# Kernel tuning notes

Measured on AMD Instinct MI355X. Metric: run time of the kernel, lower is better.

Reference implementation:

```python
import jax, jax.numpy as jnp
import numpy as np

LAMBDA_REG = 0.1
EPS = 1e-05


def setup_inputs() -> dict:
    key = jax.random.key(0)
    k1, k2, k3 = jax.random.split(key, 3)
    D, DIM, N = 32, 16, 4096
    A_real = jax.random.normal(k1, (D, DIM, DIM), dtype=jnp.float32)
    A_imag = jax.random.normal(k2, (D, DIM, DIM), dtype=jnp.float32)
    X = jax.random.normal(k3, (N, D), dtype=jnp.float32)
    return {"A_real": A_real, "A_imag": A_imag, "X": X}


def reference(A_real, A_imag, X):
    # A: [D, dim, dim] complex operators; X: [N, D] real positions
    A = (A_real + 1j * A_imag).astype(jnp.complex64)
    N, D = X.shape
    dim = A.shape[-1]
    Xc = X.astype(jnp.complex64)
    I = jnp.eye(dim, dtype=jnp.complex64)

    valid = jnp.isfinite(Xc)                      # [N, D]
    valid_e = valid[:, :, None, None]             # [N, D, 1, 1]
    scaled_I = Xc[:, :, None, None] * I           # [N, D, dim, dim]
    A_exp = A[None, :, :, :]                      # [1, D, dim, dim] (broadcast over N)
    scaled_I_clean = jnp.where(valid_e, scaled_I, A_exp)
    H_diff = jnp.where(valid_e, A_exp - scaled_I_clean, 0.0)  # [N, D, dim, dim]

    # 0.5 * sum_d H_diff @ H_diff^H  (Hermitian by construction)
    H = 0.5 * jnp.einsum('ndij,ndkj->nik', H_diff, jnp.conj(H_diff))
    H = H + EPS * I                               # [N, dim, dim]

    eigvals, eigvecs = jnp.linalg.eigh(H)
    psi0 = eigvecs[:, :, 0]                       # ground state, [N, dim]
    phase = psi0[:, 0] / jnp.abs(psi0[:, 0])
    psi0 = psi0 / phase[:, None]
    projector = psi0[:, :, None] * jnp.conj(psi0)[:, None, :]  # [N, dim, dim]

    # Faithful to torch.einsum('ndij,njk->nd', ...): sums over i, j AND k
    position = jnp.einsum('dij,njk->nd', A, projector).real    # [N, D]
    A2 = jnp.matmul(A, A)                                       # [D, dim, dim]
    expectation_A2 = jnp.einsum('dij,njk->nd', A2, projector).real
    variance = jnp.sum(expectation_A2 - position ** 2)

    position_error = jnp.sum((position - X) ** 2)
    loss = (position_error + LAMBDA_REG * variance) / N
    return loss
```

## Files before the change

kernel.cpp:

```cpp
#include <hip/hip_runtime.h>

#define NS 4096
#define DC 32
#define MAXROUND 210
#define CHKIV 8

typedef float v2f __attribute__((ext_vector_type(2)));

#define CFENCE() asm volatile("" ::: "memory")

static __device__ __forceinline__ v2f vswap(v2f b) {
    return __builtin_shufflevector(b, b, 1, 0);
}

static __device__ __forceinline__ float dpp_from_hi(float x) {
    return __int_as_float(__builtin_amdgcn_update_dpp(
        0, __float_as_int(x), 0x101, 0xf, 0xf, true));
}
static __device__ __forceinline__ float dpp_from_lo(float x) {
    return __int_as_float(__builtin_amdgcn_update_dpp(
        0, __float_as_int(x), 0x111, 0xf, 0xf, true));
}
static __device__ __forceinline__ v2f dpp2_from_hi(v2f v) {
    return (v2f){dpp_from_hi(v.x), dpp_from_hi(v.y)};
}
static __device__ __forceinline__ v2f dpp2_from_lo(v2f v) {
    return (v2f){dpp_from_lo(v.x), dpp_from_lo(v.y)};
}

static __device__ __forceinline__ int slot_of(int r, int rr) {
    if (r == 15) return 0;
    int m = r - rr; if (m < 0) m += 15;
    if (m == 0) return 1;
    return (m <= 7) ? 2*m : 31 - 2*m;
}
static __device__ __forceinline__ int pi_next(int s) {
    if (s == 0) return 0;
    if (s == 2) return 1;
    if (!(s & 1)) return s - 2;
    return (s == 15) ? 14 : s + 2;
}
static __device__ __forceinline__ int kmix(int sr) {
    return ((sr >> 1) ^ ((sr & 1) << 2)) & 7;
}
static __device__ __forceinline__ int laddr(int sr, int sc) {
    return (sr << 7) | ((((sc >> 1) ^ kmix(sr)) & 7) << 4) | ((sc & 1) << 3);
}

static __device__ __forceinline__ float4 make_rot(float4 f0, float4 f1) {
    float av = f0.x, dv = f1.z;
    float ab2 = f0.z*f0.z + f0.w*f0.w;
    float c_, s_, er, ei;
    if (ab2 > 1e-60f) {
        float abr = __builtin_amdgcn_rsqf(ab2);
        er = f0.z * abr; ei = f0.w * abr;
        float tau = (dv - av) * (0.5f * abr);
        float den = fabsf(tau) + sqrtf(1.f + tau*tau);
        float tv = __builtin_amdgcn_rcpf(den);
        tv = (tau < 0.f) ? -tv : tv;
        c_ = __builtin_amdgcn_rsqf(1.f + tv*tv);
        s_ = tv * c_;
    } else { c_ = 1.f; s_ = 0.f; er = 1.f; ei = 0.f; }
    return make_float4(c_, s_, er, ei);
}

static __device__ __forceinline__ void rot_quartet(
    float4 fa, float4 fb,
    float4 f0, float4 f1, v2f q11, v2f q12, v2f q21, v2f q22,
    v2f& n11, v2f& n12, v2f& n21, v2f& n22,
    v2f& u11, v2f& u12, v2f& u21, v2f& u22)
{
    v2f h11 = {f0.x, f0.y}, h12 = {f0.z, f0.w};
    v2f h21 = {f1.x, f1.y}, h22 = {f1.z, f1.w};

    const float cb = fb.x, sb = fb.y, ebx = fb.z, eby = fb.w;
    const float sbex = sb*ebx, sbey = sb*eby;
    const float cbex = cb*ebx, cbey = cb*eby;
    const v2f CB  = {cb, cb},      SB  = {sb, sb};
    const v2f P1x = {-sbex,-sbex}, P1y = {-sbey, sbey};
    const v2f Q1x = {cbex, cbex},  Q1y = {cbey,-cbey};
    const float ca = fa.x, sa = fa.y, eax = fa.z, eay = fa.w;
    const float saex = sa*eax, saey = sa*eay;
    const float caex = ca*eax, caey = ca*eay;
    const v2f CA  = {ca, ca},      SA  = {sa, sa};
    const v2f P2x = {-saex,-saex}, P2y = {saey,-saey};
    const v2f Q2x = {caex, caex},  Q2y = {-caey, caey};

    v2f t11 = CB*h11  + P1x*h12 + P1y*vswap(h12);
    v2f t12 = Q1x*h12 + Q1y*vswap(h12) + SB*h11;
    v2f t21 = CB*h21  + P1x*h22 + P1y*vswap(h22);
    v2f t22 = Q1x*h22 + Q1y*vswap(h22) + SB*h21;
    n11 = CA*t11  + P2x*t21 + P2y*vswap(t21);
    n12 = CA*t12  + P2x*t22 + P2y*vswap(t22);
    n21 = Q2x*t21 + Q2y*vswap(t21) + SA*t11;
    n22 = Q2x*t22 + Q2y*vswap(t22) + SA*t12;
    u11 = CB*q11  + P1x*q12 + P1y*vswap(q12);
    u12 = Q1x*q12 + Q1y*vswap(q12) + SB*q11;
    u21 = CB*q21  + P1x*q22 + P1y*vswap(q22);
    u22 = Q1x*q22 + Q1y*vswap(q22) + SB*q21;
}

static __device__ __forceinline__ void v_advance(
    bool b0, bool b7,
    v2f u11, v2f u12, v2f u21, v2f u22,
    v2f& q11, v2f& q12, v2f& q21, v2f& q22)
{
    v2f s11 = dpp2_from_hi(u11);
    v2f s21 = dpp2_from_hi(u21);
    v2f l12 = dpp2_from_lo(u12);
    v2f l22 = dpp2_from_lo(u22);
    q11 = b7 ? u12 : (b0 ? u11 : s11);
    q21 = b7 ? u22 : (b0 ? u21 : s21);
    q12 = b0 ? s11 : l12;
    q22 = b0 ? s21 : l22;
}

__global__ __launch_bounds__(256) void precompute_kernel(
    const float* __restrict__ Ar, const float* __restrict__ Ai,
    float2* __restrict__ S, float2* __restrict__ W,
    float2* __restrict__ cA, float2* __restrict__ cA2,
    float* __restrict__ out)
{
    const int d = blockIdx.x;
    const int t = threadIdx.x;
    if (d == 0 && t == 0) out[0] = 0.f;
    const int i = t >> 4, j = t & 15;
    __shared__ float ar[16][16], ai[16][16], a2r[16][16], a2i[16][16];
    ar[i][j] = Ar[d*256 + t];
    ai[i][j] = Ai[d*256 + t];
    __syncthreads();
    float a2re = 0.f, a2im = 0.f, wre = 0.f, wim = 0.f;
    for (int k = 0; k < 16; ++k) {
        float xr = ar[i][k], xi = ai[i][k];
        a2re += xr*ar[k][j] - xi*ai[k][j];
        a2im += xr*ai[k][j] + xi*ar[k][j];
        wre += xr*ar[j][k] + xi*ai[j][k];
        wim += xi*ar[j][k] - xr*ai[j][k];
    }
    S[d*256 + t] = make_float2(ar[i][j] + ar[j][i], ai[i][j] - ai[j][i]);
    W[d*256 + t] = make_float2(wre, wim);
    a2r[i][j] = a2re; a2i[i][j] = a2im;
    __syncthreads();
    if (t < 16) {
        float sr = 0.f, si = 0.f, s2r = 0.f, s2i = 0.f;
        for (int ii = 0; ii < 16; ++ii) {
            sr  += ar[ii][t];  si  += ai[ii][t];
            s2r += a2r[ii][t]; s2i += a2i[ii][t];
        }
        cA [d*16 + t] = make_float2(sr,  si);
        cA2[d*16 + t] = make_float2(s2r, s2i);
    }
}

__global__ __launch_bounds__(64) void energy_kernel(
    const float* __restrict__ X,
    const float2* __restrict__ S, const float2* __restrict__ W,
    const float2* __restrict__ cA, const float2* __restrict__ cA2,
    float* __restrict__ out)
{
    const int n0 = blockIdx.x * 2;
    const int t = threadIdx.x;
    const int a = t >> 3, b = t & 7;

    __shared__ __align__(16) v2f H[2][256];
    __shared__ float4 csco[2][8];
    __shared__ float4 vS[2][16][8];
    __shared__ float  xS[2][32];
    __shared__ float  diagS[2][16];
    __shared__ v2f    psiS[2][16];
    __shared__ int    midxS[2];

    const float* XA = X + n0*DC;
    const float* XB = X + (n0 + 1)*DC;
    if (t < 32) { xS[0][t] = XA[t]; xS[1][t] = XB[t]; }

    const int sr0 = 2*a, sr1 = 2*a + 1;
    const int sc0 = 2*b, sc1 = 2*b + 1;
    const int rd0 = (sr0 << 7) | (((b ^ kmix(sr0)) & 7) << 4);
    const int rd1 = (sr1 << 7) | (((b ^ kmix(sr1)) & 7) << 4);
    const int pr0 = pi_next(sr0), pr1 = pi_next(sr1);
    const int pc0 = pi_next(sc0), pc1 = pi_next(sc1);
    const int wH00 = laddr(pr0, pc0), wH01 = laddr(pr0, pc1);
    const int wH10 = laddr(pr1, pc0), wH11 = laddr(pr1, pc1);
    const bool diagLane = (a == b);
    const bool b0 = (b == 0), b7 = (b == 7);

    const int j0 = b0 ? 15 : b;
    const int j1 = b0 ? 0  : 15 - b;
    v2f qA11 = {(sr0 == j0) ? 1.f : 0.f, 0.f};
    v2f qA12 = {(sr0 == j1) ? 1.f : 0.f, 0.f};
    v2f qA21 = {(sr1 == j0) ? 1.f : 0.f, 0.f};
    v2f qA22 = {(sr1 == j1) ? 1.f : 0.f, 0.f};
    v2f qB11 = qA11, qB12 = qA12, qB21 = qA21, qB22 = qA22;

    float invTolA, invTolB;
    {
        const int bi = t >> 2, bj = (t & 3) * 4, e0 = t * 4;
        v2f accA[4] = {{0.f,0.f},{0.f,0.f},{0.f,0.f},{0.f,0.f}};
        v2f accB[4] = {{0.f,0.f},{0.f,0.f},{0.f,0.f},{0.f,0.f}};
        float sxa = 0.f, sxb = 0.f;
        for (int d = 0; d < DC; ++d) {
            float xa = XA[d], xb = XB[d];
            sxa += xa*xa; sxb += xb*xb;
            const float4* w4 = (const float4*)(W + d*256 + e0);
            const float4* s4 = (const float4*)(S + d*256 + e0);
            float4 wa = w4[0], wb = w4[1];
            float4 sa = s4[0], sb = s4[1];
            v2f xva = {xa, xa}, xvb = {xb, xb};
            accA[0] += (v2f){wa.x, wa.y} - xva * (v2f){sa.x, sa.y};
            accA[1] += (v2f){wa.z, wa.w} - xva * (v2f){sa.z, sa.w};
            accA[2] += (v2f){wb.x, wb.y} - xva * (v2f){sb.x, sb.y};
            accA[3] += (v2f){wb.z, wb.w} - xva * (v2f){sb.z, sb.w};
            accB[0] += (v2f){wa.x, wa.y} - xvb * (v2f){sa.x, sa.y};
            accB[1] += (v2f){wa.z, wa.w} - xvb * (v2f){sa.z, sa.w};
            accB[2] += (v2f){wb.x, wb.y} - xvb * (v2f){sb.x, sb.y};
            accB[3] += (v2f){wb.z, wb.w} - xvb * (v2f){sb.z, sb.w};
        }
        float sdA = 0.5f*sxa + 1e-5f;
        float sdB = 0.5f*sxb + 1e-5f;
        float nfA = 0.f, nfB = 0.f;
        const int sbi = slot_of(bi, 0);
        #pragma unroll
        for (int u = 0; u < 4; ++u) {
            int j = bj + u;
            v2f hA = 0.5f * accA[u];
            v2f hB = 0.5f * accB[u];
            if (bi == j) { hA.x += sdA; hB.x += sdB; }
            nfA += hA.x*hA.x + hA.y*hA.y;
            nfB += hB.x*hB.x + hB.y*hB.y;
            const int scj = slot_of(j, 0);
            *(v2f*)((char*)H + laddr(sbi, scj)) = hA;
            *(v2f*)((char*)H + 2048 + laddr(sbi, scj)) = hB;
        }
        #pragma unroll
        for (int m = 1; m < 64; m <<= 1) {
            nfA += __shfl_xor(nfA, m);
            nfB += __shfl_xor(nfB, m);
        }
        invTolA = __builtin_amdgcn_rcpf(1e-10f * nfA);
        invTolB = __builtin_amdgcn_rcpf(1e-10f * nfB);
    }
    __syncthreads();

    int rr = 0, iter = 0, chkcd = CHKIV;
    for (;;) {
        const char* Hc = (const char*)H;
        float4 f0A = *(const float4*)(Hc + rd0);
        float4 f1A = *(const float4*)(Hc + rd1);
        float4 f0B = *(const float4*)(Hc + 2048 + rd0);
        float4 f1B = *(const float4*)(Hc + 2048 + rd1);

        if (diagLane) {
            csco[0][a] = make_rot(f0A, f1A);
            csco[1][a] = make_rot(f0B, f1B);
        }
        CFENCE();

        float4 faA = csco[0][a], fbA = csco[0][b];
        float4 faB = csco[1][a], fbB = csco[1][b];

        v2f n11A, n12A, n21A, n22A, u11A, u12A, u21A, u22A;
        v2f n11B, n12B, n21B, n22B, u11B, u12B, u21B, u22B;
        rot_quartet(faA, fbA, f0A, f1A, qA11, qA12, qA21, qA22,
                    n11A, n12A, n21A, n22A, u11A, u12A, u21A, u22A);
        rot_quartet(faB, fbB, f0B, f1B, qB11, qB12, qB21, qB22,
                    n11B, n12B, n21B, n22B, u11B, u12B, u21B, u22B);

        char* Hw = (char*)H;
        *(v2f*)(Hw + wH00) = n11A;
        *(v2f*)(Hw + wH01) = n12A;
        *(v2f*)(Hw + wH10) = n21A;
        *(v2f*)(Hw + wH11) = n22A;
        *(v2f*)(Hw + 2048 + wH00) = n11B;
        *(v2f*)(Hw + 2048 + wH01) = n12B;
        *(v2f*)(Hw + 2048 + wH10) = n21B;
        *(v2f*)(Hw + 2048 + wH11) = n22B;

        v_advance(b0, b7, u11A, u12A, u21A, u22A, qA11, qA12, qA21, qA22);
        v_advance(b0, b7, u11B, u12B, u21B, u22B, qB11, qB12, qB21, qB22);
        CFENCE();

        rr = (rr == 14) ? 0 : rr + 1;
        ++iter;
        if (chkcd == 1) {
            float oA = n12A.x*n12A.x + n12A.y*n12A.y + n21A.x*n21A.x + n21A.y*n21A.y;
            float oB = n12B.x*n12B.x + n12B.y*n12B.y + n21B.x*n21B.x + n21B.y*n21B.y;
            if (!diagLane) {
                oA += n11A.x*n11A.x + n11A.y*n11A.y + n22A.x*n22A.x + n22A.y*n22A.y;
                oB += n11B.x*n11B.x + n11B.y*n11B.y + n22B.x*n22B.x + n22B.y*n22B.y;
            }
            oA *= invTolA; oB *= invTolB;
            #pragma unroll
            for (int m = 1; m < 64; m <<= 1) {
                oA += __shfl_xor(oA, m);
                oB += __shfl_xor(oB, m);
            }
            if (fmaxf(oA, oB) < 1.f || iter >= MAXROUND) break;
            chkcd = CHKIV;
        } else { --chkcd; }
    }

    vS[0][sr0][b] = make_float4(qA11.x, qA11.y, qA12.x, qA12.y);
    vS[0][sr1][b] = make_float4(qA21.x, qA21.y, qA22.x, qA22.y);
    vS[1][sr0][b] = make_float4(qB11.x, qB11.y, qB12.x, qB12.y);
    vS[1][sr1][b] = make_float4(qB21.x, qB21.y, qB22.x, qB22.y);
    __syncthreads();

    const int rrx = rr;
    if (t < 32) {
        const int s = t >> 4, r = t & 15;
        const int sd = slot_of(r, rrx);
        diagS[s][r] = (*(const v2f*)((const char*)H + s*2048 + laddr(sd, sd))).x;
    }
    __syncthreads();
    if ((t & 31) == 0) {
        const int s = t >> 5;
        float best = diagS[s][0]; int bi_ = 0;
        for (int m = 1; m < 16; ++m) {
            float vv = diagS[s][m];
            if (vv < best) { best = vv; bi_ = m; }
        }
        midxS[s] = bi_;
    }
    __syncthreads();
    if (t < 32) {
        const int s = t >> 4, r = t & 15;
        const int sm = slot_of(midxS[s], rrx);
        float4 f4 = vS[s][r][sm >> 1];
        psiS[s][r] = (sm & 1) ? (v2f){f4.z, f4.w} : (v2f){f4.x, f4.y};
    }
    __syncthreads();

    float contrib;
    {
        const int s = t >> 5, d = t & 31;
        float tr = 0.f, ti = 0.f;
        v2f psi[16];
        for (int jj = 0; jj < 16; ++jj) {
            psi[jj] = psiS[s][jj];
            tr += psi[jj].x; ti += psi[jj].y;
        }
        float zr = 0.f, zi = 0.f, z2r = 0.f, z2i = 0.f;
        for (int jj = 0; jj < 16; ++jj) {
            float2 cj  = cA [d*16 + jj];
            float2 c2j = cA2[d*16 + jj];
            zr  += cj.x*psi[jj].x  - cj.y*psi[jj].y;
            zi  += cj.x*psi[jj].y  + cj.y*psi[jj].x;
            z2r += c2j.x*psi[jj].x - c2j.y*psi[jj].y;
            z2i += c2j.x*psi[jj].y + c2j.y*psi[jj].x;
        }
        float pos = zr*tr + zi*ti;
        float e2  = z2r*tr + z2i*ti;
        float dx  = pos - xS[s][d];
        contrib = dx*dx + 0.1f*(e2 - pos*pos);
    }
    #pragma unroll
    for (int m = 1; m < 64; m <<= 1)
        contrib += __shfl_xor(contrib, m);
    if (t == 0) atomicAdd(out, contrib * (1.0f/(float)NS));
}

extern "C" void kernel_launch(void* const* d_in, const int* in_sizes, int n_in,
                              void* d_out, int out_size, void* d_ws, size_t ws_size,
                              hipStream_t stream)
{
    const float* A_real = (const float*)d_in[0];
    const float* A_imag = (const float*)d_in[1];
    const float* X      = (const float*)d_in[2];
    float* out = (float*)d_out;

    float2* S   = (float2*)d_ws;
    float2* W   = S  + DC*256;
    float2* cA  = W  + DC*256;
    float2* cA2 = cA + DC*16;
    (void)in_sizes; (void)n_in; (void)out_size; (void)ws_size;

    precompute_kernel<<<DC, 256, 0, stream>>>(A_real, A_imag, S, W, cA, cA2, out);
    energy_kernel<<<NS/2, 64, 0, stream>>>(X, S, W, cA, cA2, out);
}
```

Baseline: 143.5 us.

## Compute Jacobi rotations redundantly per lane from compact pivot buffer

Rather than having diagonal lanes compute rotation parameters and publish them through shared memory for the other lanes to read, the kernel now keeps a compact per-pair buffer (diagonals plus off-diagonal element) in LDS. The lanes that produce the next step's pivot entries write it, and every lane computes its own row and column rotations redundantly. This removes a serialized dependency: rotation compute on a few lanes followed by an LDS round trip inside each sweep step. The cost is more redundant transcendental math per lane and extra conditional LDS stores.

```diff
diff --git a/kernel.cpp b/kernel.cpp
--- a/kernel.cpp
+++ b/kernel.cpp
@@ -47,13 +47,13 @@
     return (sr << 7) | ((((sc >> 1) ^ kmix(sr)) & 7) << 4) | ((sc & 1) << 3);
 }
 
-static __device__ __forceinline__ float4 make_rot(float4 f0, float4 f1) {
-    float av = f0.x, dv = f1.z;
-    float ab2 = f0.z*f0.z + f0.w*f0.w;
+static __device__ __forceinline__ float4 make_rotq(float4 d) {
+    float av = d.z, dv = d.w;
+    float ab2 = d.x*d.x + d.y*d.y;
     float c_, s_, er, ei;
     if (ab2 > 1e-60f) {
         float abr = __builtin_amdgcn_rsqf(ab2);
-        er = f0.z * abr; ei = f0.w * abr;
+        er = d.x * abr; ei = d.y * abr;
         float tau = (dv - av) * (0.5f * abr);
         float den = fabsf(tau) + sqrtf(1.f + tau*tau);
         float tv = __builtin_amdgcn_rcpf(den);
@@ -163,7 +163,7 @@
     const int a = t >> 3, b = t & 7;
 
     __shared__ __align__(16) v2f H[2][256];
-    __shared__ float4 csco[2][8];
+    __shared__ __align__(16) float4 Dq[2][8];
     __shared__ float4 vS[2][16][8];
     __shared__ float  xS[2][32];
     __shared__ float  diagS[2][16];
@@ -184,6 +184,18 @@
     const int wH10 = laddr(pr1, pc0), wH11 = laddr(pr1, pc1);
     const bool diagLane = (a == b);
     const bool b0 = (b == 0), b7 = (b == 7);
+
+    const bool dg00 = (pr0 == pc0), dg01 = (pr0 == pc1);
+    const bool dg10 = (pr1 == pc0), dg11 = (pr1 == pc1);
+    const bool of00 = (!(pr0 & 1)) && (pc0 == pr0 + 1);
+    const bool of01 = (!(pr0 & 1)) && (pc1 == pr0 + 1);
+    const bool of10 = (!(pr1 & 1)) && (pc0 == pr1 + 1);
+    const bool of11 = (!(pr1 & 1)) && (pc1 == pr1 + 1);
+    const int  dof0 = (pr0 >> 1)*16 + ((pr0 & 1) ? 12 : 8);
+    const int  dof1 = (pr1 >> 1)*16 + ((pr1 & 1) ? 12 : 8);
+    const int  oof0 = (pr0 >> 1)*16;
+    const int  oof1 = (pr1 >> 1)*16;
+    char* DqB = (char*)Dq;
 
     const int j0 = b0 ? 15 : b;
     const int j1 = b0 ? 0  : 15 - b;
@@ -231,6 +243,16 @@
             const int scj = slot_of(j, 0);
             *(v2f*)((char*)H + laddr(sbi, scj)) = hA;
             *(v2f*)((char*)H + 2048 + laddr(sbi, scj)) = hB;
+            if (sbi == scj) {
+                int off = (sbi >> 1)*16 + ((sbi & 1) ? 12 : 8);
+                *(float*)(DqB + off)       = hA.x;
+                *(float*)(DqB + 128 + off) = hB.x;
+            }
+            if (!(sbi & 1) && (scj == sbi + 1)) {
+                int off = (sbi >> 1)*16;
+                *(v2f*)(DqB + off)       = hA;
+                *(v2f*)(DqB + 128 + off) = hB;
+            }
         }
         #pragma unroll
         for (int m = 1; m < 64; m <<= 1) {
@@ -249,15 +271,12 @@
         float4 f1A = *(const float4*)(Hc + rd1);
         float4 f0B = *(const float4*)(Hc + 2048 + rd0);
         float4 f1B = *(const float4*)(Hc + 2048 + rd1);
-
-        if (diagLane) {
-            csco[0][a] = make_rot(f0A, f1A);
-            csco[1][a] = make_rot(f0B, f1B);
-        }
-        CFENCE();
-
-        float4 faA = csco[0][a], fbA = csco[0][b];
-        float4 faB = csco[1][a], fbB = csco[1][b];
+        const float4* Dq4 = (const float4*)Dq;
+        float4 dqaA = Dq4[a],     dqbA = Dq4[b];
+        float4 dqaB = Dq4[8 + a], dqbB = Dq4[8 + b];
+
+        float4 faA = make_rotq(dqaA), fbA = make_rotq(dqbA);
+        float4 faB = make_rotq(dqaB), fbB = make_rotq(dqbB);
 
         v2f n11A, n12A, n21A, n22A, u11A, u12A, u21A, u22A;
         v2f n11B, n12B, n21B, n22B, u11B, u12B, u21B, u22B;
@@ -275,6 +294,15 @@
         *(v2f*)(Hw + 2048 + wH01) = n12B;
         *(v2f*)(Hw + 2048 + wH10) = n21B;
         *(v2f*)(Hw + 2048 + wH11) = n22B;
+
+        if (dg00) { *(float*)(DqB + dof0) = n11A.x; *(float*)(DqB + 128 + dof0) = n11B.x; }
+        if (dg01) { *(float*)(DqB + dof0) = n12A.x; *(float*)(DqB + 128 + dof0) = n12B.x; }
+        if (dg10) { *(float*)(DqB + dof1) = n21A.x; *(float*)(DqB + 128 + dof1) = n21B.x; }
+        if (dg11) { *(float*)(DqB + dof1) = n22A.x; *(float*)(DqB + 128 + dof1) = n22B.x; }
+        if (of00) { *(v2f*)(DqB + oof0) = n11A; *(v2f*)(DqB + 128 + oof0) = n11B; }
+        if (of01) { *(v2f*)(DqB + oof0) = n12A; *(v2f*)(DqB + 128 + oof0) = n12B; }
+        if (of10) { *(v2f*)(DqB + oof1) = n21A; *(v2f*)(DqB + 128 + oof1) = n21B; }
+        if (of11) { *(v2f*)(DqB + oof1) = n22A; *(v2f*)(DqB + 128 + oof1) = n22B; }
 
         v_advance(b0, b7, u11A, u12A, u21A, u22A, qA11, qA12, qA21, qA22);
         v_advance(b0, b7, u11B, u12B, u21B, u22B, qB11, qB12, qB21, qB22);
```

Result: slower. 172.6 us (+20.2%).
